# Performance work log

Measured on AMD Instinct MI355X. Metric: run time of the kernel, lower is better.

Reference implementation:

```python
import jax, jax.numpy as jnp
import numpy as np

TEMPERATURE = 8.0

def setup_inputs() -> dict:
    key = jax.random.key(0)
    kq, kk, kv, km = jax.random.split(key, 4)
    B, H, S, D = 4, 16, 2048, 64
    q = jax.random.normal(kq, (B, H, S, D), dtype=jnp.float32)
    k = jax.random.normal(kk, (B, H, S, D), dtype=jnp.float32)
    v = jax.random.normal(kv, (B, H, S, D), dtype=jnp.float32)
    mask = jax.random.randint(km, (B, S, S), 0, 2, dtype=jnp.int32)
    return {"q": q, "k": k, "v": v, "mask": mask}

def reference(q, k, v, mask):
    # attn = q @ k^T / temperature  -> [B, H, Sq, Sk]
    attn = jnp.einsum("bhqd,bhkd->bhqk", q, k) / TEMPERATURE
    mask0 = (mask == 0)[:, None, :, :]  # [B, 1, Sq, Sk]; True where masked out
    attn = jnp.where(mask0, -jnp.inf, attn)
    attn = jax.nn.softmax(attn, axis=-1)
    attn = jnp.where(mask0, 0.0, attn)
    output = jnp.einsum("bhqk,bhkd->bhqd", attn, v)
    return (output, attn)
```

## Files before the change

### kernel.cpp

```cpp
#include <hip/hip_runtime.h>
#include <cstdint>

#define B_ 4
#define H_ 16
#define S_ 2048
#define D_ 64

#define QSCALE (0.125f * 1.44269504088896f)

typedef _Float16 half8 __attribute__((ext_vector_type(8)));
typedef float f32x4 __attribute__((ext_vector_type(4)));
typedef float f32x16 __attribute__((ext_vector_type(16)));
typedef uint32_t u32x2 __attribute__((ext_vector_type(2)));
typedef uint32_t u32x4 __attribute__((ext_vector_type(4)));


__global__ void cvt_q_kernel(const float* __restrict__ q, _Float16* __restrict__ qh) {
    const int64_t N = (int64_t)B_ * H_ * S_ * D_;
    const int64_t step = (int64_t)gridDim.x * blockDim.x * 4;
    for (int64_t i = ((int64_t)blockIdx.x * blockDim.x + threadIdx.x) * 4; i < N; i += step) {
        float4 a = *reinterpret_cast<const float4*>(q + i);
        _Float16 ah[4] = { (_Float16)(a.x * QSCALE), (_Float16)(a.y * QSCALE),
                           (_Float16)(a.z * QSCALE), (_Float16)(a.w * QSCALE) };
        *reinterpret_cast<u32x2*>(qh + i) = *reinterpret_cast<u32x2*>(ah);
    }
}

__global__ void pack_k_kernel(const float* __restrict__ k, _Float16* __restrict__ kh) {
    const int bh = blockIdx.y;
    const int t = blockIdx.x;
    const int tid = threadIdx.x;
    const int kk = tid >> 6, lane = tid & 63, hi = lane >> 5, c = lane & 31;
    const float* src = k + ((int64_t)bh * S_ + t * 32 + c) * D_ + kk * 16 + hi * 8;
    float4 a = *reinterpret_cast<const float4*>(src);
    float4 b2 = *reinterpret_cast<const float4*>(src + 4);
    half8 h = { (_Float16)a.x, (_Float16)a.y, (_Float16)a.z, (_Float16)a.w,
                (_Float16)b2.x, (_Float16)b2.y, (_Float16)b2.z, (_Float16)b2.w };
    half8* dst = reinterpret_cast<half8*>(kh) + (((int64_t)bh * 64 + t) * 4 + kk) * 64 + hi * 32 + c;
    *dst = h;
}

__global__ void pack_v_kernel(const float* __restrict__ v, _Float16* __restrict__ vt) {
    const int bh = blockIdx.y;
    const int t = blockIdx.x;
    const int tid = threadIdx.x;
    const int g = tid >> 5, c = tid & 31;
    const int kk = g >> 2, hi = (g >> 1) & 1, db = g & 1;
    const float* src = v + ((int64_t)bh * S_ + t * 32 + kk * 16 + hi * 8) * D_ + c + 32 * db;
    half8 h;
#pragma unroll
    for (int j = 0; j < 8; ++j) h[j] = (_Float16)src[j * D_];
    half8* dst = reinterpret_cast<half8*>(vt) + (((int64_t)bh * 64 + t) * 8 + g) * 32 + c;
    *dst = h;
}

__global__ void pack_mask_kernel(const int* __restrict__ mask, uint32_t* __restrict__ mbT) {
    const int64_t groups = (int64_t)B_ * S_ * S_ / 64;
    const int lane = threadIdx.x & 63;
    const int64_t wstep = ((int64_t)gridDim.x * blockDim.x) >> 6;
    for (int64_t g = ((int64_t)blockIdx.x * blockDim.x + threadIdx.x) >> 6; g < groups; g += wstep) {
        int mv = mask[g * 64 + lane];
        unsigned long long bits = __ballot(mv != 0);
        if (lane == 0) {
            const int u = (int)(g & 31);
            const int64_t bq = g >> 5;
            const int q = (int)(bq & (S_ - 1));
            const int b = (int)(bq >> 11);
            const int64_t base = (((int64_t)b * 64 + (q >> 5)) * 64) * 32 + (q & 31);
            mbT[base + (int64_t)(2 * u) * 32]     = (uint32_t)bits;
            mbT[base + (int64_t)(2 * u + 1) * 32] = (uint32_t)(bits >> 32);
        }
    }
}


__global__ __launch_bounds__(256, 2) void attn_fast(
    const _Float16* __restrict__ qh, const _Float16* __restrict__ kh, const _Float16* __restrict__ vt,
    const uint32_t* __restrict__ mbT,
    float* __restrict__ out, float* __restrict__ attn)
{
    const int tid = threadIdx.x;
    const int w = tid >> 6;
    const int lane = tid & 63;
    const int c = lane & 31;
    const int hi = lane >> 5;

    const int fid = blockIdx.x;
    const int xcd = fid & 7;
    const int slot = fid >> 3;
    const int p = xcd + 8 * (slot >> 4);
    const int x = slot & 15;
    const int b = p >> 4;

    const int qw = x * 128 + w * 32;
    const int64_t bh = p;

    half8 aq[4];
    {
        const _Float16* qp = qh + (bh * S_ + qw + c) * D_ + hi * 8;
#pragma unroll
        for (int kk = 0; kk < 4; ++kk)
            aq[kk] = *reinterpret_cast<const half8*>(qp + kk * 16);
    }

    const uint32_t* mT = mbT + (((int64_t)b * 64 + x * 4 + w) * 64) * 32 + c;
    const half8* kbase = reinterpret_cast<const half8*>(kh) + (int64_t)bh * 64 * 4 * 64 + hi * 32 + c;
    const half8* vbase = reinterpret_cast<const half8*>(vt) + (int64_t)bh * 64 * 8 * 32 + c;

    auto LOADK = [&](half8 (&kr)[4], int t) {
        const half8* kp8 = kbase + (int64_t)t * 256;
#pragma unroll
        for (int kk = 0; kk < 4; ++kk) kr[kk] = kp8[kk * 64];
    };
    auto LOADV = [&](half8 (&vr)[4], int t) {
        const half8* vp8 = vbase + (int64_t)t * 256;
        vr[0] = vp8[(hi * 2 + 0) * 32];
        vr[1] = vp8[(hi * 2 + 1) * 32];
        vr[2] = vp8[(4 + hi * 2 + 0) * 32];
        vr[3] = vp8[(4 + hi * 2 + 1) * 32];
    };
    auto QK = [&](const half8 (&kr)[4]) -> f32x16 {
        f32x16 acc;
#pragma unroll
        for (int r = 0; r < 16; ++r) acc[r] = 0.f;
#pragma unroll
        for (int kk = 0; kk < 4; ++kk)
            acc = __builtin_amdgcn_mfma_f32_32x32x16_f16(kr[kk], aq[kk], acc, 0, 0, 0);
        return acc;
    };

    float l = 0.f;
    {
        auto bodyA = [&](const half8 (&kr)[4], uint32_t mwf) -> float {
            f32x16 acc = QK(kr);
            const uint32_t mw = mwf >> (hi * 4);
            float e[16];
#pragma unroll
            for (int r = 0; r < 16; ++r) {
                const bool dead = ((mw >> ((r & 3) + 8 * (r >> 2))) & 1u) == 0u;
                e[r] = __builtin_exp2f(dead ? -1e30f : acc[r]);
            }
#pragma unroll
            for (int st = 1; st < 16; st <<= 1)
#pragma unroll
                for (int i = 0; i < 16; i += 2 * st) e[i] += e[i + st];
            return e[0];
        };

        half8 k0_[4], k1_[4], k2_[4], k3_[4];
        uint32_t m0, m1, m2, m3;
        LOADK(k0_, 0); m0 = mT[0 * 32];
        LOADK(k1_, 1); m1 = mT[1 * 32];
        LOADK(k2_, 2); m2 = mT[2 * 32];
        LOADK(k3_, 3); m3 = mT[3 * 32];
        for (int t = 0; t < 64; t += 4) {
            l += bodyA(k0_, m0); if (t + 4 < 64) { LOADK(k0_, t + 4); m0 = mT[(t + 4) * 32]; }
            l += bodyA(k1_, m1); if (t + 5 < 64) { LOADK(k1_, t + 5); m1 = mT[(t + 5) * 32]; }
            l += bodyA(k2_, m2); if (t + 6 < 64) { LOADK(k2_, t + 6); m2 = mT[(t + 6) * 32]; }
            l += bodyA(k3_, m3); if (t + 7 < 64) { LOADK(k3_, t + 7); m3 = mT[(t + 7) * 32]; }
        }
    }
    const float lt = l + __shfl_xor(l, 32);
    const float rinv = 1.0f / lt;

    f32x16 o0, o1;
#pragma unroll
    for (int r = 0; r < 16; ++r) { o0[r] = 0.f; o1[r] = 0.f; }

    {
        auto stepB = [&](half8 (&K)[4], half8 (&V)[4], uint32_t& m_, int t, int tn) {
            const int k0 = t * 32;
            f32x16 acc = QK(K);
            const uint32_t mw = m_ >> (hi * 4);

            f32x4 pq0, pq1, pq2, pq3;
            uint32_t pk[8];
#pragma unroll
            for (int e2 = 0; e2 < 4; ++e2) {
                bool d0 = ((mw >> (0 + e2)) & 1u) == 0u;
                bool d1 = ((mw >> (8 + e2)) & 1u) == 0u;
                bool d2 = ((mw >> (16 + e2)) & 1u) == 0u;
                bool d3 = ((mw >> (24 + e2)) & 1u) == 0u;
                pq0[e2] = __builtin_exp2f(d0 ? -1e30f : acc[e2]) * rinv;
                pq1[e2] = __builtin_exp2f(d1 ? -1e30f : acc[4 + e2]) * rinv;
                pq2[e2] = __builtin_exp2f(d2 ? -1e30f : acc[8 + e2]) * rinv;
                pq3[e2] = __builtin_exp2f(d3 ? -1e30f : acc[12 + e2]) * rinv;
            }
            pk[0] = __builtin_bit_cast(uint32_t, __builtin_amdgcn_cvt_pkrtz(pq0[0], pq0[1]));
            pk[1] = __builtin_bit_cast(uint32_t, __builtin_amdgcn_cvt_pkrtz(pq0[2], pq0[3]));
            pk[2] = __builtin_bit_cast(uint32_t, __builtin_amdgcn_cvt_pkrtz(pq1[0], pq1[1]));
            pk[3] = __builtin_bit_cast(uint32_t, __builtin_amdgcn_cvt_pkrtz(pq1[2], pq1[3]));
            pk[4] = __builtin_bit_cast(uint32_t, __builtin_amdgcn_cvt_pkrtz(pq2[0], pq2[1]));
            pk[5] = __builtin_bit_cast(uint32_t, __builtin_amdgcn_cvt_pkrtz(pq2[2], pq2[3]));
            pk[6] = __builtin_bit_cast(uint32_t, __builtin_amdgcn_cvt_pkrtz(pq3[0], pq3[1]));
            pk[7] = __builtin_bit_cast(uint32_t, __builtin_amdgcn_cvt_pkrtz(pq3[2], pq3[3]));

            u32x2 rA = __builtin_amdgcn_permlane32_swap(pk[0], pk[2], false, false);
            u32x2 rB = __builtin_amdgcn_permlane32_swap(pk[1], pk[3], false, false);
            u32x2 rC = __builtin_amdgcn_permlane32_swap(pk[4], pk[6], false, false);
            u32x2 rD = __builtin_amdgcn_permlane32_swap(pk[5], pk[7], false, false);
            u32x4 fa0 = { rA[0], rB[0], rA[1], rB[1] };
            u32x4 fa1 = { rC[0], rD[0], rC[1], rD[1] };
            half8 pa0 = __builtin_bit_cast(half8, fa0);
            half8 pa1 = __builtin_bit_cast(half8, fa1);

            o0 = __builtin_amdgcn_mfma_f32_32x32x16_f16(pa0, V[0], o0, 0, 0, 0);
            o1 = __builtin_amdgcn_mfma_f32_32x32x16_f16(pa0, V[1], o1, 0, 0, 0);
            o0 = __builtin_amdgcn_mfma_f32_32x32x16_f16(pa1, V[2], o0, 0, 0, 0);
            o1 = __builtin_amdgcn_mfma_f32_32x32x16_f16(pa1, V[3], o1, 0, 0, 0);

            if (tn < 64) { LOADK(K, tn); LOADV(V, tn); m_ = mT[tn * 32]; }

            float* arow = attn + (bh * S_ + qw + c) * (int64_t)S_ + k0 + 4 * hi;
            *reinterpret_cast<f32x4*>(arow) = pq0;
            *reinterpret_cast<f32x4*>(arow + 8) = pq1;
            *reinterpret_cast<f32x4*>(arow + 16) = pq2;
            *reinterpret_cast<f32x4*>(arow + 24) = pq3;
        };

        half8 Ka[4], Kb[4], Kc[4], Va[4], Vb[4], Vc[4];
        uint32_t ma, mb_, mc;
        LOADK(Ka, 0); LOADV(Va, 0); ma = mT[0 * 32];
        LOADK(Kb, 1); LOADV(Vb, 1); mb_ = mT[1 * 32];
        LOADK(Kc, 2); LOADV(Vc, 2); mc = mT[2 * 32];
        for (int t = 0; t < 63; t += 3) {
            stepB(Ka, Va, ma, t, t + 3);
            stepB(Kb, Vb, mb_, t + 1, t + 4);
            stepB(Kc, Vc, mc, t + 2, t + 5);
        }
        stepB(Ka, Va, ma, 63, 64);
    }

#pragma unroll
    for (int r = 0; r < 16; ++r) {
        const int row = (r & 3) + 8 * (r >> 2) + 4 * hi;
        float* op = out + (bh * S_ + qw + row) * D_;
        op[c] = o0[r];
        op[c + 32] = o1[r];
    }
}

__global__ __launch_bounds__(256, 2) void attn_slow(
    const float* __restrict__ qf, const float* __restrict__ kf, const float* __restrict__ vf,
    const int* __restrict__ maskI, float* __restrict__ out, float* __restrict__ attn)
{
    const int tid = threadIdx.x;
    const int w = tid >> 6;
    const int lane = tid & 63;
    const int c = lane & 31;
    const int hi = lane >> 5;
    const int fid = blockIdx.x;
    const int p = fid & 63;
    const int x = fid >> 6;
    const int b = p >> 4;
    const int qw = x * 128 + w * 32;
    const int64_t bh = p;
    const int64_t qrow = (int64_t)b * S_ + qw + c;

    half8 aq[4];
    {
        const float* qp = qf + (bh * S_ + qw + c) * D_ + hi * 8;
#pragma unroll
        for (int kk = 0; kk < 4; ++kk)
#pragma unroll
            for (int j = 0; j < 8; ++j)
                aq[kk][j] = (_Float16)(qp[kk * 16 + j] * QSCALE);
    }

    float l = 0.f;
    for (int t = 0; t < 64; ++t) {
        const int k0 = t * 32;
        f32x16 acc;
#pragma unroll
        for (int r = 0; r < 16; ++r) acc[r] = 0.f;
        const float* kp = kf + (bh * S_ + k0 + c) * D_ + hi * 8;
#pragma unroll
        for (int kk = 0; kk < 4; ++kk) {
            half8 bk;
#pragma unroll
            for (int j = 0; j < 8; ++j) bk[j] = (_Float16)kp[kk * 16 + j];
            acc = __builtin_amdgcn_mfma_f32_32x32x16_f16(bk, aq[kk], acc, 0, 0, 0);
        }
        float e[16];
#pragma unroll
        for (int r = 0; r < 16; ++r) {
            const int key = k0 + (r & 3) + 8 * (r >> 2) + 4 * hi;
            const bool dead = maskI[qrow * S_ + key] == 0;
            e[r] = __builtin_exp2f(dead ? -1e30f : acc[r]);
        }
#pragma unroll
        for (int st = 1; st < 16; st <<= 1)
#pragma unroll
            for (int i = 0; i < 16; i += 2 * st) e[i] += e[i + st];
        l += e[0];
    }
    const float lt = l + __shfl_xor(l, 32);
    const float rinv = 1.0f / lt;

    f32x16 o0, o1;
#pragma unroll
    for (int r = 0; r < 16; ++r) { o0[r] = 0.f; o1[r] = 0.f; }

    for (int t = 0; t < 64; ++t) {
        const int k0 = t * 32;
        f32x16 acc;
#pragma unroll
        for (int r = 0; r < 16; ++r) acc[r] = 0.f;
        const float* kp = kf + (bh * S_ + k0 + c) * D_ + hi * 8;
#pragma unroll
        for (int kk = 0; kk < 4; ++kk) {
            half8 bk;
#pragma unroll
            for (int j = 0; j < 8; ++j) bk[j] = (_Float16)kp[kk * 16 + j];
            acc = __builtin_amdgcn_mfma_f32_32x32x16_f16(bk, aq[kk], acc, 0, 0, 0);
        }
        float* arow = attn + (bh * S_ + qw + c) * (int64_t)S_ + k0 + 4 * hi;
        uint32_t pk[8];
#pragma unroll
        for (int g4 = 0; g4 < 4; ++g4) {
            f32x4 pq;
#pragma unroll
            for (int e2 = 0; e2 < 4; ++e2) {
                const int key = k0 + e2 + 8 * g4 + 4 * hi;
                const bool dead = maskI[qrow * S_ + key] == 0;
                pq[e2] = __builtin_exp2f(dead ? -1e30f : acc[4 * g4 + e2]) * rinv;
            }
            *reinterpret_cast<f32x4*>(arow + 8 * g4) = pq;
            pk[2 * g4]     = __builtin_bit_cast(uint32_t, __builtin_amdgcn_cvt_pkrtz(pq[0], pq[1]));
            pk[2 * g4 + 1] = __builtin_bit_cast(uint32_t, __builtin_amdgcn_cvt_pkrtz(pq[2], pq[3]));
        }
        u32x2 rA = __builtin_amdgcn_permlane32_swap(pk[0], pk[2], false, false);
        u32x2 rB = __builtin_amdgcn_permlane32_swap(pk[1], pk[3], false, false);
        u32x2 rC = __builtin_amdgcn_permlane32_swap(pk[4], pk[6], false, false);
        u32x2 rD = __builtin_amdgcn_permlane32_swap(pk[5], pk[7], false, false);
        u32x4 fa0 = { rA[0], rB[0], rA[1], rB[1] };
        u32x4 fa1 = { rC[0], rD[0], rC[1], rD[1] };
        half8 pa0 = __builtin_bit_cast(half8, fa0);
        half8 pa1 = __builtin_bit_cast(half8, fa1);

        half8 bv00, bv01, bv10, bv11;
        const float* vp0 = vf + (bh * S_ + k0 + hi * 8) * D_ + c;
        const float* vp1 = vp0 + 16 * D_;
#pragma unroll
        for (int j = 0; j < 8; ++j) {
            bv00[j] = (_Float16)vp0[j * D_];
            bv01[j] = (_Float16)vp0[j * D_ + 32];
            bv10[j] = (_Float16)vp1[j * D_];
            bv11[j] = (_Float16)vp1[j * D_ + 32];
        }
        o0 = __builtin_amdgcn_mfma_f32_32x32x16_f16(pa0, bv00, o0, 0, 0, 0);
        o1 = __builtin_amdgcn_mfma_f32_32x32x16_f16(pa0, bv01, o1, 0, 0, 0);
        o0 = __builtin_amdgcn_mfma_f32_32x32x16_f16(pa1, bv10, o0, 0, 0, 0);
        o1 = __builtin_amdgcn_mfma_f32_32x32x16_f16(pa1, bv11, o1, 0, 0, 0);
    }

#pragma unroll
    for (int r = 0; r < 16; ++r) {
        const int row = (r & 3) + 8 * (r >> 2) + 4 * hi;
        float* op = out + (bh * S_ + qw + row) * D_;
        op[c] = o0[r];
        op[c + 32] = o1[r];
    }
}

extern "C" void kernel_launch(void* const* d_in, const int* in_sizes, int n_in,
                              void* d_out, int out_size, void* d_ws, size_t ws_size,
                              hipStream_t stream) {
    const float* q = (const float*)d_in[0];
    const float* k = (const float*)d_in[1];
    const float* v = (const float*)d_in[2];
    const int* mask = (const int*)d_in[3];
    float* out = (float*)d_out;
    float* attn = out + (int64_t)B_ * H_ * S_ * D_;

    const size_t nElem = (size_t)B_ * H_ * S_ * D_;
    const size_t maskWords = (size_t)B_ * S_ * (S_ / 32);
    const size_t need = nElem * 2 * 3 + maskWords * 4;

    const int nblk = B_ * H_ * (S_ / 128);
    if (d_ws != nullptr && ws_size >= need) {
        _Float16* qh = (_Float16*)d_ws;
        _Float16* kh = qh + nElem;
        _Float16* vt = kh + nElem;
        uint32_t* mbT = (uint32_t*)(vt + nElem);
        cvt_q_kernel<<<1024, 256, 0, stream>>>(q, qh);
        pack_k_kernel<<<dim3(S_ / 32, B_ * H_), 256, 0, stream>>>(k, kh);
        pack_v_kernel<<<dim3(S_ / 32, B_ * H_), 256, 0, stream>>>(v, vt);
        pack_mask_kernel<<<2048, 256, 0, stream>>>(mask, mbT);
        attn_fast<<<nblk, 256, 0, stream>>>(qh, kh, vt, mbT, out, attn);
    } else {
        attn_slow<<<nblk, 256, 0, stream>>>(q, k, v, mask, out, attn);
    }
}
```

Before: 545.4 us.

## Shrink prefetch depth to cut registers and raise occupancy to four blocks

Raises the launch bound from 2 to 4 blocks per CU. To fit that register budget, the pass-1 K prefetch ring drops from four buffers to two and the pass-2 K/V ring from three buffers to two. V is no longer prefetched a tile ahead: it is loaded inside the current step just before the PV MFMAs. The aim is to hide memory latency through more resident waves instead of deep software pipelining. The cost is exposed V load latency within each step, and possible spills if the compiler cannot fit the halved budget.

```diff
diff --git a/kernel.cpp b/kernel.cpp
--- a/kernel.cpp
+++ b/kernel.cpp
@@ -74,7 +74,7 @@
 }
 
 
-__global__ __launch_bounds__(256, 2) void attn_fast(
+__global__ __launch_bounds__(256, 4) void attn_fast(
     const _Float16* __restrict__ qh, const _Float16* __restrict__ kh, const _Float16* __restrict__ vt,
     const uint32_t* __restrict__ mbT,
     float* __restrict__ out, float* __restrict__ attn)
@@ -112,13 +112,6 @@
 #pragma unroll
         for (int kk = 0; kk < 4; ++kk) kr[kk] = kp8[kk * 64];
     };
-    auto LOADV = [&](half8 (&vr)[4], int t) {
-        const half8* vp8 = vbase + (int64_t)t * 256;
-        vr[0] = vp8[(hi * 2 + 0) * 32];
-        vr[1] = vp8[(hi * 2 + 1) * 32];
-        vr[2] = vp8[(4 + hi * 2 + 0) * 32];
-        vr[3] = vp8[(4 + hi * 2 + 1) * 32];
-    };
     auto QK = [&](const half8 (&kr)[4]) -> f32x16 {
         f32x16 acc;
 #pragma unroll
@@ -147,17 +140,14 @@
             return e[0];
         };
 
-        half8 k0_[4], k1_[4], k2_[4], k3_[4];
-        uint32_t m0, m1, m2, m3;
-        LOADK(k0_, 0); m0 = mT[0 * 32];
-        LOADK(k1_, 1); m1 = mT[1 * 32];
-        LOADK(k2_, 2); m2 = mT[2 * 32];
-        LOADK(k3_, 3); m3 = mT[3 * 32];
-        for (int t = 0; t < 64; t += 4) {
-            l += bodyA(k0_, m0); if (t + 4 < 64) { LOADK(k0_, t + 4); m0 = mT[(t + 4) * 32]; }
-            l += bodyA(k1_, m1); if (t + 5 < 64) { LOADK(k1_, t + 5); m1 = mT[(t + 5) * 32]; }
-            l += bodyA(k2_, m2); if (t + 6 < 64) { LOADK(k2_, t + 6); m2 = mT[(t + 6) * 32]; }
-            l += bodyA(k3_, m3); if (t + 7 < 64) { LOADK(k3_, t + 7); m3 = mT[(t + 7) * 32]; }
+        half8 ka[4], kb[4];
+        uint32_t ma, mb_;
+        LOADK(ka, 0); ma = mT[0];
+        for (int t = 0; t < 64; t += 2) {
+            LOADK(kb, t + 1); mb_ = mT[(t + 1) * 32];
+            l += bodyA(ka, ma);
+            if (t + 2 < 64) { LOADK(ka, t + 2); ma = mT[(t + 2) * 32]; }
+            l += bodyA(kb, mb_);
         }
     }
     const float lt = l + __shfl_xor(l, 32);
@@ -168,10 +158,21 @@
     for (int r = 0; r < 16; ++r) { o0[r] = 0.f; o1[r] = 0.f; }
 
     {
-        auto stepB = [&](half8 (&K)[4], half8 (&V)[4], uint32_t& m_, int t, int tn) {
+        auto stepB = [&](half8 (&K)[4], uint32_t& m_, int t, int tn) {
             const int k0 = t * 32;
             f32x16 acc = QK(K);
             const uint32_t mw = m_ >> (hi * 4);
+
+            if (tn < 64) { LOADK(K, tn); m_ = mT[tn * 32]; }
+
+            half8 V0, V1, V2, V3;
+            {
+                const half8* vp8 = vbase + (int64_t)t * 256;
+                V0 = vp8[(hi * 2 + 0) * 32];
+                V1 = vp8[(hi * 2 + 1) * 32];
+                V2 = vp8[(4 + hi * 2 + 0) * 32];
+                V3 = vp8[(4 + hi * 2 + 1) * 32];
+            }
 
             f32x4 pq0, pq1, pq2, pq3;
             uint32_t pk[8];
@@ -204,12 +205,10 @@
             half8 pa0 = __builtin_bit_cast(half8, fa0);
             half8 pa1 = __builtin_bit_cast(half8, fa1);
 
-            o0 = __builtin_amdgcn_mfma_f32_32x32x16_f16(pa0, V[0], o0, 0, 0, 0);
-            o1 = __builtin_amdgcn_mfma_f32_32x32x16_f16(pa0, V[1], o1, 0, 0, 0);
-            o0 = __builtin_amdgcn_mfma_f32_32x32x16_f16(pa1, V[2], o0, 0, 0, 0);
-            o1 = __builtin_amdgcn_mfma_f32_32x32x16_f16(pa1, V[3], o1, 0, 0, 0);
-
-            if (tn < 64) { LOADK(K, tn); LOADV(V, tn); m_ = mT[tn * 32]; }
+            o0 = __builtin_amdgcn_mfma_f32_32x32x16_f16(pa0, V0, o0, 0, 0, 0);
+            o1 = __builtin_amdgcn_mfma_f32_32x32x16_f16(pa0, V1, o1, 0, 0, 0);
+            o0 = __builtin_amdgcn_mfma_f32_32x32x16_f16(pa1, V2, o0, 0, 0, 0);
+            o1 = __builtin_amdgcn_mfma_f32_32x32x16_f16(pa1, V3, o1, 0, 0, 0);
 
             float* arow = attn + (bh * S_ + qw + c) * (int64_t)S_ + k0 + 4 * hi;
             *reinterpret_cast<f32x4*>(arow) = pq0;
@@ -218,17 +217,14 @@
             *reinterpret_cast<f32x4*>(arow + 24) = pq3;
         };
 
-        half8 Ka[4], Kb[4], Kc[4], Va[4], Vb[4], Vc[4];
-        uint32_t ma, mb_, mc;
-        LOADK(Ka, 0); LOADV(Va, 0); ma = mT[0 * 32];
-        LOADK(Kb, 1); LOADV(Vb, 1); mb_ = mT[1 * 32];
-        LOADK(Kc, 2); LOADV(Vc, 2); mc = mT[2 * 32];
-        for (int t = 0; t < 63; t += 3) {
-            stepB(Ka, Va, ma, t, t + 3);
-            stepB(Kb, Vb, mb_, t + 1, t + 4);
-            stepB(Kc, Vc, mc, t + 2, t + 5);
-        }
-        stepB(Ka, Va, ma, 63, 64);
+        half8 Ka[4], Kb[4];
+        uint32_t ma, mb_;
+        LOADK(Ka, 0); ma = mT[0];
+        LOADK(Kb, 1); mb_ = mT[1 * 32];
+        for (int t = 0; t < 64; t += 2) {
+            stepB(Ka, ma, t, t + 2);
+            stepB(Kb, mb_, t + 1, t + 3);
+        }
     }
 
 #pragma unroll
```

Result: slower. 708.1 us (+29.8%).
